# Performance work log

Measured on AMD Instinct MI355X. Metric: run time of the kernel, lower is better.

## Reference

```python
import jax, jax.numpy as jnp
import numpy as np
from jax import lax

LEAK = 0.2   # LeakyReLU negative slope
EPS = 1e-5   # LayerNorm eps (torch default)
K = 16       # nsample

def _lrelu(x):
    return jnp.where(x > 0, x, LEAK * x)

def _ln(x, g, b):
    m = x.mean(-1, keepdims=True)
    v = x.var(-1, keepdims=True)
    return (x - m) / jnp.sqrt(v + EPS) * g + b

def _pointconv(xyz, new_xyz, feats, W, b):
    # xyz [B,N,3], new_xyz [B,M,3], feats [B,N,C] -> [B,M,O]
    d2 = (jnp.sum(new_xyz**2, -1)[:, :, None]
          + jnp.sum(xyz**2, -1)[:, None, :]
          - 2.0 * jnp.einsum('bmd,bnd->bmn', new_xyz, xyz))   # [B,M,N]
    _, idx = lax.top_k(-d2, K)                                # kNN indices [B,M,K]
    bidx = jnp.arange(xyz.shape[0])[:, None, None]
    g_xyz = xyz[bidx, idx] - new_xyz[:, :, None, :]           # relative coords [B,M,K,3]
    g_f = feats[bidx, idx]                                    # neighbor feats  [B,M,K,C]
    g = jnp.concatenate([g_xyz, g_f], -1)                     # [B,M,K,C+3]
    h = _lrelu(jnp.einsum('bmkc,co->bmko', g, W) + b)         # local MLP
    return h.max(2)                                           # max-pool over neighbors

def setup_inputs():
    key = jax.random.key(0)
    ks = jax.random.split(key, 8)
    B, N, base, C1 = 256, 1024, 16, 32
    def w(k, shape, fan):
        return jax.random.normal(k, shape, jnp.float32) * (1.0 / np.sqrt(fan))
    return dict(
        point_cloud=jax.random.normal(ks[0], (B, 3, N), jnp.float32),
        pw_W0=w(ks[1], (3, base), 3), pw_b0=jnp.zeros(base), pw_g0=jnp.ones(base), pw_beta0=jnp.zeros(base),
        pw_W1=w(ks[2], (base, base), base), pw_b1=jnp.zeros(base), pw_g1=jnp.ones(base), pw_beta1=jnp.zeros(base),
        pc0_W=w(ks[3], (base + 3, C1), base + 3), pc0_b=jnp.zeros(C1),
        bn_Ws=w(ks[4], (C1, C1 // 4), C1), bn_bs=jnp.zeros(C1 // 4),
        bn_Wc=w(ks[5], (C1 // 4 + 3, 128), C1 // 4 + 3), bn_bc=jnp.zeros(128),
        bn_We=w(ks[6], (128, 256), 128), bn_be=jnp.zeros(256),
    )

def reference(point_cloud, pw_W0, pw_b0, pw_g0, pw_beta0, pw_W1, pw_b1, pw_g1, pw_beta1,
              pc0_W, pc0_b, bn_Ws, bn_bs, bn_Wc, bn_bc, bn_We, bn_be):
    xyz0 = jnp.swapaxes(point_cloud, 1, 2)   # [B,1024,3]
    xyz1 = xyz0[:, ::2]                      # strided downsample -> [B,512,3]
    xyz2 = xyz1[:, ::4]                      # -> [B,128,3]
    # pointwise MLP (Linear-LN-LeakyReLU x2)
    f = _lrelu(_ln(xyz0 @ pw_W0 + pw_b0, pw_g0, pw_beta0))
    f = _lrelu(_ln(f @ pw_W1 + pw_b1, pw_g1, pw_beta1))       # [B,1024,16]
    # PointConv layer 0: 1024 -> 512 points, 16 -> 32 ch
    f = _pointconv(xyz0, xyz1, f, pc0_W, pc0_b)               # [B,512,32]
    # BottleneckStridedPointConv: squeeze (32->8), grouped conv (->128), expand (->256)
    fs = _lrelu(f @ bn_Ws + bn_bs)                            # [B,512,8]
    f = _pointconv(xyz1, xyz2, fs, bn_Wc, bn_bc)              # [B,128,128]
    f = f @ bn_We + bn_be                                     # [B,128,256]
    return f.mean(1)                                          # mean over points -> [B,256]
```

## Files before the change

kernel.cpp:

```cpp
#include <hip/hip_runtime.h>
#include <float.h>
#include <math.h>

#define LEAK 0.2f
#define EPS 1e-5f

__device__ __forceinline__ float lrelu(float v){ return v > 0.f ? v : LEAK*v; }

__device__ __forceinline__ void ln_lrelu16(float* h, const float* __restrict__ g, const float* __restrict__ be){
  float mu = 0.f;
#pragma unroll
  for (int o=0;o<16;o++) mu += h[o];
  mu *= 0.0625f;
  float var = 0.f;
#pragma unroll
  for (int o=0;o<16;o++){ float d = h[o]-mu; var += d*d; }
  var *= 0.0625f;
  float rs = 1.0f / sqrtf(var + EPS);
#pragma unroll
  for (int o=0;o<16;o++){ float v = (h[o]-mu)*rs*g[o] + be[o]; h[o] = lrelu(v); }
}

__global__ __launch_bounds__(256) void prep_kernel(const float* __restrict__ pc,
    const float* __restrict__ W0, const float* __restrict__ b0, const float* __restrict__ g0, const float* __restrict__ be0,
    const float* __restrict__ W1, const float* __restrict__ b1, const float* __restrict__ g1, const float* __restrict__ be1,
    float4* __restrict__ cand, float* __restrict__ feats)
{
  const int p = blockIdx.x*256 + threadIdx.x;
  const int b = p >> 10, n = p & 1023;
  const float* base = pc + b*3072;
  const float x = base[n], y = base[1024+n], z = base[2048+n];
  cand[p] = make_float4(x, y, z, x*x + y*y + z*z);
  float h[16];
#pragma unroll
  for (int o=0;o<16;o++) h[o] = b0[o] + x*W0[o] + y*W0[16+o] + z*W0[32+o];
  ln_lrelu16(h, g0, be0);
  float h2[16];
#pragma unroll
  for (int o=0;o<16;o++){
    float s = b1[o];
#pragma unroll
    for (int c=0;c<16;c++) s += h[c]*W1[c*16+o];
    h2[o] = s;
  }
  ln_lrelu16(h2, g1, be1);
  float4* fo = (float4*)(feats + p*16);
  fo[0] = make_float4(h2[0],h2[1],h2[2],h2[3]);
  fo[1] = make_float4(h2[4],h2[5],h2[6],h2[7]);
  fo[2] = make_float4(h2[8],h2[9],h2[10],h2[11]);
  fo[3] = make_float4(h2[12],h2[13],h2[14],h2[15]);
}

#define KNN_SENT 0xFF7FFC00u
__device__ __forceinline__ unsigned enc_key(float d, int n){
  unsigned u = __float_as_uint(d);
  u ^= (unsigned)(((int)u) >> 31) | 0x80000000u;
  return (u & ~1023u) | (unsigned)n;
}
__device__ __forceinline__ float dec_key(unsigned k){
  unsigned u = k ^ ((unsigned)(~(((int)k) >> 31)) | 0x80000000u);
  return __uint_as_float(u);
}

__device__ __forceinline__ unsigned med3u(unsigned a, unsigned b, unsigned c){
  unsigned d;
  asm("v_med3_u32 %0, %1, %2, %3" : "=v"(d) : "v"(a), "v"(b), "v"(c));
  return d;
}

__device__ __forceinline__ void ins_sorted(unsigned (&dk)[16], unsigned key){
#pragma unroll
  for (int j=15;j>0;--j) dk[j] = med3u(dk[j-1], dk[j], key);
  dk[0] = key < dk[0] ? key : dk[0];
}

template<int QS, int CS, int NQTOT, int NQ, int SPLIT, int NCAND>
__device__ __forceinline__ void knn_body(const float4* __restrict__ cand, int* __restrict__ idx_out)
{
  constexpr int NC = NCAND / SPLIT;
  constexpr int QG = NQTOT / NQ;
  constexpr int W  = SPLIT*NQ;
  constexpr int QSL = QS / CS;
  __shared__ unsigned md[16*W];
  __shared__ float4 scand[NCAND];
  const int b = blockIdx.x / QG, qg = blockIdx.x % QG;
  const int tid = threadIdx.x;
  const int m = tid & (NQ-1), s = tid / NQ;
  const int mg = qg*NQ + m;
  const float4* __restrict__ cb = cand + b*1024;

  for (int i = tid; i < NCAND; i += NQ*SPLIT)
    scand[i] = cb[i*CS];
  __syncthreads();

  const float4 qv = scand[mg*QSL];
  const float qx2=-2.f*qv.x, qy2=-2.f*qv.y, qz2=-2.f*qv.z;
  const int n0u = __builtin_amdgcn_readfirstlane(s*NC);

  unsigned dk[16];
#pragma unroll
  for (int j=0;j<16;j++) dk[j] = KNN_SENT;

#pragma unroll
  for (int t=0;t<16;t++){
    float4 c = scand[n0u+t];
    float d = fmaf(c.x,qx2, fmaf(c.y,qy2, fmaf(c.z,qz2, c.w)));
    ins_sorted(dk, enc_key(d, n0u+t));
  }
  float Tf = dec_key(dk[15]);

  for (int ch=0; ch<NC/64; ch++){
    const int cb0u = n0u + ch*64;
    unsigned long long msk = 0ull;
    if (ch == 0){
#pragma unroll
      for (int t=16;t<64;t++){
        float4 c = scand[cb0u+t];
        float d = fmaf(c.x,qx2, fmaf(c.y,qy2, fmaf(c.z,qz2, c.w)));
        if (d < Tf) msk |= (1ull<<t);
      }
    } else {
#pragma unroll 16
      for (int t=0;t<64;t++){
        float4 c = scand[cb0u+t];
        float d = fmaf(c.x,qx2, fmaf(c.y,qy2, fmaf(c.z,qz2, c.w)));
        if (d < Tf) msk |= (1ull<<t);
      }
    }
    while (msk){
      const int t = __builtin_ctzll(msk);
      msk &= msk-1ull;
      float4 c = scand[cb0u+t];
      float d = fmaf(c.x,qx2, fmaf(c.y,qy2, fmaf(c.z,qz2, c.w)));
      ins_sorted(dk, enc_key(d, cb0u+t));
    }
    Tf = dec_key(dk[15]);
  }

  if (s > 0){
    const int col = s*NQ + m;
#pragma unroll
    for (int j=0;j<16;j++) md[j*W + col] = dk[j];
  }
#pragma unroll
  for (int step = SPLIT/2; step > 1; step >>= 1){
    __syncthreads();
    if (s < step){
      const int col2 = (s+step)*NQ + m;
#pragma unroll
      for (int j=0;j<16;j++) ins_sorted(dk, md[j*W + col2]);
      if (s > 0){
        const int col = s*NQ + m;
#pragma unroll
        for (int j=0;j<16;j++) md[j*W + col] = dk[j];
      }
    }
  }
  __syncthreads();
  if (s == 0){
    const int col2 = NQ + m;
#pragma unroll
    for (int j=0;j<16;j++){
      unsigned o = md[(15-j)*W + col2];
      dk[j] = o < dk[j] ? o : dk[j];
    }
    int ik[16];
#pragma unroll
    for (int j=0;j<16;j++) ik[j] = (int)(dk[j] & 1023u);
    int4* op = (int4*)(idx_out + (b*NQTOT + mg)*16);
    op[0] = make_int4(ik[0],ik[1],ik[2],ik[3]);
    op[1] = make_int4(ik[4],ik[5],ik[6],ik[7]);
    op[2] = make_int4(ik[8],ik[9],ik[10],ik[11]);
    op[3] = make_int4(ik[12],ik[13],ik[14],ik[15]);
  }
}

__global__ __attribute__((amdgpu_flat_work_group_size(1024,1024), amdgpu_waves_per_eu(4,4)))
void knn1_kernel(const float4* __restrict__ cand, int* __restrict__ idx_out){
  knn_body<2,1,512,512,2,1024>(cand, idx_out);
}
__global__ __attribute__((amdgpu_flat_work_group_size(1024,1024), amdgpu_waves_per_eu(4,4)))
void knn2_kernel(const float4* __restrict__ cand, int* __restrict__ idx_out){
  knn_body<8,2,128,128,8,512>(cand, idx_out);
}

__global__ __attribute__((amdgpu_flat_work_group_size(512,512), amdgpu_waves_per_eu(4,4)))
void feat1_kernel(const float4* __restrict__ cand,
    const float* __restrict__ feats, const int* __restrict__ idx1,
    const float* __restrict__ W, const float* __restrict__ Wb,
    const float* __restrict__ Ws,
    float* __restrict__ p1part)
{
  __shared__ float sPT[16*1024];
  __shared__ float sx[1024], sy[1024], sz[1024];
  const int bx = blockIdx.x;
  const int b = bx >> 1, ob = bx & 1;
  const int ob16 = ob*16;
  const int tid = threadIdx.x;
  const float4* __restrict__ cb = cand + b*1024;
  { float4 c0 = cb[tid], c1 = cb[tid+512];
    sx[tid]=c0.x; sy[tid]=c0.y; sz[tid]=c0.z;
    sx[tid+512]=c1.x; sy[tid+512]=c1.y; sz[tid+512]=c1.z; }

  const float4* __restrict__ fb4 = (const float4*)(feats + b*16384);
#pragma unroll
  for (int i=0;i<2;i++){
    const int j = tid + i*512;
    float4 f0 = fb4[j*4+0], f1 = fb4[j*4+1], f2 = fb4[j*4+2], f3 = fb4[j*4+3];
    float f[16] = {f0.x,f0.y,f0.z,f0.w, f1.x,f1.y,f1.z,f1.w,
                   f2.x,f2.y,f2.z,f2.w, f3.x,f3.y,f3.z,f3.w};
#pragma unroll
    for (int o4=0;o4<4;o4++){
      float4 s = *(const float4*)(Wb + ob16 + o4*4);
#pragma unroll
      for (int c=0;c<16;c++){
        float4 w = *(const float4*)(W + (3+c)*32 + ob16 + o4*4);
        s.x = fmaf(f[c], w.x, s.x);
        s.y = fmaf(f[c], w.y, s.y);
        s.z = fmaf(f[c], w.z, s.z);
        s.w = fmaf(f[c], w.w, s.w);
      }
      sPT[(o4*4+0)*1024 + j] = s.x;
      sPT[(o4*4+1)*1024 + j] = s.y;
      sPT[(o4*4+2)*1024 + j] = s.z;
      sPT[(o4*4+3)*1024 + j] = s.w;
    }
  }
  __syncthreads();

  const int m = tid;
  const float qx = sx[2*m], qy = sy[2*m], qz = sz[2*m];
  int idxr[16];
  { const int4* ip = (const int4*)(idx1 + (b*512+m)*16);
    int4 a=ip[0], b2=ip[1], c2=ip[2], d2=ip[3];
    idxr[0]=a.x; idxr[1]=a.y; idxr[2]=a.z; idxr[3]=a.w;
    idxr[4]=b2.x; idxr[5]=b2.y; idxr[6]=b2.z; idxr[7]=b2.w;
    idxr[8]=c2.x; idxr[9]=c2.y; idxr[10]=c2.z; idxr[11]=c2.w;
    idxr[12]=d2.x; idxr[13]=d2.y; idxr[14]=d2.z; idxr[15]=d2.w; }

  float w0[16], w1[16], w2[16];
#pragma unroll
  for (int i=0;i<4;i++){
    float4 a = *(const float4*)(W +       ob16 + i*4);
    float4 bb= *(const float4*)(W + 32  + ob16 + i*4);
    float4 cc= *(const float4*)(W + 64  + ob16 + i*4);
    w0[i*4]=a.x; w0[i*4+1]=a.y; w0[i*4+2]=a.z; w0[i*4+3]=a.w;
    w1[i*4]=bb.x; w1[i*4+1]=bb.y; w1[i*4+2]=bb.z; w1[i*4+3]=bb.w;
    w2[i*4]=cc.x; w2[i*4+1]=cc.y; w2[i*4+2]=cc.z; w2[i*4+3]=cc.w;
  }

  float acc[16];
#pragma unroll
  for (int o=0;o<16;o++) acc[o] = -FLT_MAX;

#pragma unroll 4
  for (int k=0;k<16;k++){
    const int j = idxr[k];
    const float gx = sx[j]-qx, gy = sy[j]-qy, gz = sz[j]-qz;
    const float* pj = sPT + j;
#pragma unroll
    for (int o=0;o<16;o++){
      float p = pj[o*1024];
      float h = fmaf(gz, w2[o], fmaf(gy, w1[o], fmaf(gx, w0[o], p)));
      acc[o] = fmaxf(acc[o], fmaxf(h, 0.2f*h));
    }
  }

  float fsacc[8] = {0.f,0.f,0.f,0.f,0.f,0.f,0.f,0.f};
#pragma unroll
  for (int o=0;o<16;o++){
    const float a = acc[o];
    float4 u = *(const float4*)(Ws + (ob16+o)*8);
    float4 v = *(const float4*)(Ws + (ob16+o)*8 + 4);
    fsacc[0] = fmaf(a, u.x, fsacc[0]);
    fsacc[1] = fmaf(a, u.y, fsacc[1]);
    fsacc[2] = fmaf(a, u.z, fsacc[2]);
    fsacc[3] = fmaf(a, u.w, fsacc[3]);
    fsacc[4] = fmaf(a, v.x, fsacc[4]);
    fsacc[5] = fmaf(a, v.y, fsacc[5]);
    fsacc[6] = fmaf(a, v.z, fsacc[6]);
    fsacc[7] = fmaf(a, v.w, fsacc[7]);
  }
  float4* op = (float4*)(p1part + ((b*2+ob)*512 + m)*8);
  op[0] = make_float4(fsacc[0],fsacc[1],fsacc[2],fsacc[3]);
  op[1] = make_float4(fsacc[4],fsacc[5],fsacc[6],fsacc[7]);
}

__global__ __attribute__((amdgpu_flat_work_group_size(512,512), amdgpu_waves_per_eu(4,4)))
void feat2_kernel(const float4* __restrict__ cand,
    const float* __restrict__ p1part, const int* __restrict__ idx2,
    const float* __restrict__ Wc, const float* __restrict__ bc,
    const float* __restrict__ bs,
    float* __restrict__ p2red)
{
  __shared__ float sP2[512*32];
  __shared__ float sx[512], sy[512], sz[512];
  __shared__ float sred[32];
  const int bx = blockIdx.x;
  const int b = bx >> 2, ob = bx & 3;
  const int o_base = ob*32;
  const int tid = threadIdx.x;

  const float4* __restrict__ cb = cand + b*1024;
  { float4 c0 = cb[2*tid];
    sx[tid]=c0.x; sy[tid]=c0.y; sz[tid]=c0.z; }
  if (tid < 32) sred[tid] = 0.f;

  { const float4* __restrict__ pa4 = (const float4*)(p1part + ((b*2+0)*512 + tid)*8);
    const float4* __restrict__ pb4 = (const float4*)(p1part + ((b*2+1)*512 + tid)*8);
    float4 a0 = pa4[0], a1 = pa4[1], c0 = pb4[0], c1 = pb4[1];
    float4 s0 = *(const float4*)(bs), s1 = *(const float4*)(bs+4);
    float f[8];
    f[0]=lrelu(a0.x+c0.x+s0.x); f[1]=lrelu(a0.y+c0.y+s0.y);
    f[2]=lrelu(a0.z+c0.z+s0.z); f[3]=lrelu(a0.w+c0.w+s0.w);
    f[4]=lrelu(a1.x+c1.x+s1.x); f[5]=lrelu(a1.y+c1.y+s1.y);
    f[6]=lrelu(a1.z+c1.z+s1.z); f[7]=lrelu(a1.w+c1.w+s1.w);
    float* row = sP2 + tid*32;
    const int sw = (tid & 7);
#pragma unroll
    for (int o4=0;o4<8;o4++){
      float4 s = *(const float4*)(bc + o_base + o4*4);
#pragma unroll
      for (int c=0;c<8;c++){
        float4 w = *(const float4*)(Wc + (3+c)*128 + o_base + o4*4);
        s.x = fmaf(f[c], w.x, s.x);
        s.y = fmaf(f[c], w.y, s.y);
        s.z = fmaf(f[c], w.z, s.z);
        s.w = fmaf(f[c], w.w, s.w);
      }
      *(float4*)(row + ((o4 ^ sw) << 2)) = s;
    }
  }
  __syncthreads();

  const int m = tid >> 2, oq = tid & 3;
  const float qx = sx[4*m], qy = sy[4*m], qz = sz[4*m];
  int idxr[16];
  { const int4* ip = (const int4*)(idx2 + (b*128+m)*16);
    int4 a=ip[0], b2=ip[1], c2=ip[2], d2=ip[3];
    idxr[0]=a.x; idxr[1]=a.y; idxr[2]=a.z; idxr[3]=a.w;
    idxr[4]=b2.x; idxr[5]=b2.y; idxr[6]=b2.z; idxr[7]=b2.w;
    idxr[8]=c2.x; idxr[9]=c2.y; idxr[10]=c2.z; idxr[11]=c2.w;
    idxr[12]=d2.x; idxr[13]=d2.y; idxr[14]=d2.z; idxr[15]=d2.w; }

  float w0[8], w1[8], w2[8];
  { const int og = o_base + oq*8;
#pragma unroll
    for (int i=0;i<2;i++){
      float4 a = *(const float4*)(Wc +        og + i*4);
      float4 bb= *(const float4*)(Wc + 128  + og + i*4);
      float4 cc= *(const float4*)(Wc + 256  + og + i*4);
      w0[i*4]=a.x; w0[i*4+1]=a.y; w0[i*4+2]=a.z; w0[i*4+3]=a.w;
      w1[i*4]=bb.x; w1[i*4+1]=bb.y; w1[i*4+2]=bb.z; w1[i*4+3]=bb.w;
      w2[i*4]=cc.x; w2[i*4+1]=cc.y; w2[i*4+2]=cc.z; w2[i*4+3]=cc.w;
    } }

  float acc[8];
#pragma unroll
  for (int o=0;o<8;o++) acc[o] = -FLT_MAX;

#pragma unroll 4
  for (int k=0;k<16;k++){
    const int j = idxr[k];
    const float gx = sx[j]-qx, gy = sy[j]-qy, gz = sz[j]-qz;
    const float* row = sP2 + j*32;
    const int sw = (j & 7);
    float4 p0 = *(const float4*)(row + (((2*oq  ) ^ sw) << 2));
    float4 p1 = *(const float4*)(row + (((2*oq+1) ^ sw) << 2));
    float h0 = fmaf(gz, w2[0], fmaf(gy, w1[0], fmaf(gx, w0[0], p0.x)));
    float h1 = fmaf(gz, w2[1], fmaf(gy, w1[1], fmaf(gx, w0[1], p0.y)));
    float h2 = fmaf(gz, w2[2], fmaf(gy, w1[2], fmaf(gx, w0[2], p0.z)));
    float h3 = fmaf(gz, w2[3], fmaf(gy, w1[3], fmaf(gx, w0[3], p0.w)));
    float h4 = fmaf(gz, w2[4], fmaf(gy, w1[4], fmaf(gx, w0[4], p1.x)));
    float h5 = fmaf(gz, w2[5], fmaf(gy, w1[5], fmaf(gx, w0[5], p1.y)));
    float h6 = fmaf(gz, w2[6], fmaf(gy, w1[6], fmaf(gx, w0[6], p1.z)));
    float h7 = fmaf(gz, w2[7], fmaf(gy, w1[7], fmaf(gx, w0[7], p1.w)));
    acc[0] = fmaxf(acc[0], fmaxf(h0, 0.2f*h0));
    acc[1] = fmaxf(acc[1], fmaxf(h1, 0.2f*h1));
    acc[2] = fmaxf(acc[2], fmaxf(h2, 0.2f*h2));
    acc[3] = fmaxf(acc[3], fmaxf(h3, 0.2f*h3));
    acc[4] = fmaxf(acc[4], fmaxf(h4, 0.2f*h4));
    acc[5] = fmaxf(acc[5], fmaxf(h5, 0.2f*h5));
    acc[6] = fmaxf(acc[6], fmaxf(h6, 0.2f*h6));
    acc[7] = fmaxf(acc[7], fmaxf(h7, 0.2f*h7));
  }

#pragma unroll
  for (int o=0;o<8;o++){
    float v = acc[o];
    v += __shfl_xor(v, 4);
    v += __shfl_xor(v, 8);
    v += __shfl_xor(v, 16);
    v += __shfl_xor(v, 32);
    if ((threadIdx.x & 60) == 0)
      atomicAdd(&sred[oq*8+o], v);
  }
  __syncthreads();
  if (tid < 32) p2red[b*128 + o_base + tid] = sred[tid];
}

__global__ __launch_bounds__(256) void final_kernel(const float* __restrict__ p2red,
    const float* __restrict__ We, const float* __restrict__ beF, float* __restrict__ out)
{
  const int b = blockIdx.x, o = threadIdx.x;
  const float* __restrict__ r0 = p2red + b*128;
  float s = 0.f;
#pragma unroll 8
  for (int c=0;c<128;c++) s += r0[c]*We[c*256+o];
  out[b*256+o] = beF[o] + s*0.0078125f;
}

extern "C" void kernel_launch(void* const* d_in, const int* in_sizes, int n_in,
                              void* d_out, int out_size, void* d_ws, size_t ws_size,
                              hipStream_t stream) {
  (void)in_sizes; (void)n_in; (void)out_size; (void)ws_size;
  const float* pc   = (const float*)d_in[0];
  const float* W0   = (const float*)d_in[1];
  const float* b0   = (const float*)d_in[2];
  const float* g0   = (const float*)d_in[3];
  const float* be0  = (const float*)d_in[4];
  const float* W1   = (const float*)d_in[5];
  const float* b1   = (const float*)d_in[6];
  const float* g1   = (const float*)d_in[7];
  const float* be1  = (const float*)d_in[8];
  const float* pcW  = (const float*)d_in[9];
  const float* pcb  = (const float*)d_in[10];
  const float* Ws   = (const float*)d_in[11];
  const float* bs   = (const float*)d_in[12];
  const float* Wc   = (const float*)d_in[13];
  const float* bc   = (const float*)d_in[14];
  const float* We   = (const float*)d_in[15];
  const float* beF  = (const float*)d_in[16];

  char* ws = (char*)d_ws;
  float4* cand0 = (float4*)ws;
  float*  feats = (float*)(ws + (4u<<20));
  float*  p2red = (float*)(ws + (4u<<20));
  int*    idx1  = (int*)  (ws + (20u<<20));
  int*    idx2  = (int*)  (ws + (28u<<20));
  float*  p1part= (float*)(ws + (30u<<20));
  float*  out   = (float*)d_out;

  prep_kernel<<<1024, 256, 0, stream>>>(pc, W0,b0,g0,be0, W1,b1,g1,be1, cand0, feats);
  knn1_kernel<<<256, 1024, 0, stream>>>(cand0, idx1);
  knn2_kernel<<<256, 1024, 0, stream>>>(cand0, idx2);
  feat1_kernel<<<512, 512, 0, stream>>>(cand0, feats, idx1, pcW, pcb, Ws, p1part);
  feat2_kernel<<<1024, 512, 0, stream>>>(cand0, p1part, idx2, Wc, bc, bs, p2red);
  final_kernel<<<256, 256, 0, stream>>>(p2red, We, beF, out);
}
```

Measured before the change: 238.5 us.

## Fuse both kNN launches into one kernel and seed top-k with 64 candidates

Merges the two kNN kernels into a single 512-block launch that dispatches by block index, sharing one statically sized LDS buffer. This removes a launch boundary and lets the two workloads run concurrently to fill the GPU. It also seeds the sorted list with the first 64 candidates via full insertion instead of 16 plus a mask pass, and relaxes the waves-per-EU hint. The shared 80KB LDS allocation is larger than what knn2 needed alone, which may reduce occupancy for those blocks. The longer seeding phase also adds insertion work.

Measured after the change: 213.5 us. 10.5% less time.

```diff
diff --git a/kernel.cpp b/kernel.cpp
--- a/kernel.cpp
+++ b/kernel.cpp
@@ -75,15 +75,14 @@
 }
 
 template<int QS, int CS, int NQTOT, int NQ, int SPLIT, int NCAND>
-__device__ __forceinline__ void knn_body(const float4* __restrict__ cand, int* __restrict__ idx_out)
+__device__ __forceinline__ void knn_body(unsigned* md, float4* scand,
+    const float4* __restrict__ cand, int bid, int* __restrict__ idx_out)
 {
   constexpr int NC = NCAND / SPLIT;
   constexpr int QG = NQTOT / NQ;
   constexpr int W  = SPLIT*NQ;
   constexpr int QSL = QS / CS;
-  __shared__ unsigned md[16*W];
-  __shared__ float4 scand[NCAND];
-  const int b = blockIdx.x / QG, qg = blockIdx.x % QG;
+  const int b = bid / QG, qg = bid % QG;
   const int tid = threadIdx.x;
   const int m = tid & (NQ-1), s = tid / NQ;
   const int mg = qg*NQ + m;
@@ -101,31 +100,22 @@
 #pragma unroll
   for (int j=0;j<16;j++) dk[j] = KNN_SENT;
 
-#pragma unroll
-  for (int t=0;t<16;t++){
+#pragma unroll 8
+  for (int t=0;t<64;t++){
     float4 c = scand[n0u+t];
     float d = fmaf(c.x,qx2, fmaf(c.y,qy2, fmaf(c.z,qz2, c.w)));
     ins_sorted(dk, enc_key(d, n0u+t));
   }
   float Tf = dec_key(dk[15]);
 
-  for (int ch=0; ch<NC/64; ch++){
+  for (int ch=1; ch<NC/64; ch++){
     const int cb0u = n0u + ch*64;
     unsigned long long msk = 0ull;
-    if (ch == 0){
-#pragma unroll
-      for (int t=16;t<64;t++){
-        float4 c = scand[cb0u+t];
-        float d = fmaf(c.x,qx2, fmaf(c.y,qy2, fmaf(c.z,qz2, c.w)));
-        if (d < Tf) msk |= (1ull<<t);
-      }
-    } else {
 #pragma unroll 16
-      for (int t=0;t<64;t++){
-        float4 c = scand[cb0u+t];
-        float d = fmaf(c.x,qx2, fmaf(c.y,qy2, fmaf(c.z,qz2, c.w)));
-        if (d < Tf) msk |= (1ull<<t);
-      }
+    for (int t=0;t<64;t++){
+      float4 c = scand[cb0u+t];
+      float d = fmaf(c.x,qx2, fmaf(c.y,qy2, fmaf(c.z,qz2, c.w)));
+      if (d < Tf) msk |= (1ull<<t);
     }
     while (msk){
       const int t = __builtin_ctzll(msk);
@@ -175,13 +165,20 @@
   }
 }
 
-__global__ __attribute__((amdgpu_flat_work_group_size(1024,1024), amdgpu_waves_per_eu(4,4)))
-void knn1_kernel(const float4* __restrict__ cand, int* __restrict__ idx_out){
-  knn_body<2,1,512,512,2,1024>(cand, idx_out);
-}
-__global__ __attribute__((amdgpu_flat_work_group_size(1024,1024), amdgpu_waves_per_eu(4,4)))
-void knn2_kernel(const float4* __restrict__ cand, int* __restrict__ idx_out){
-  knn_body<8,2,128,128,8,512>(cand, idx_out);
+__global__ __attribute__((amdgpu_flat_work_group_size(1024,1024), amdgpu_waves_per_eu(4,8)))
+void knn_fused_kernel(const float4* __restrict__ cand,
+                      int* __restrict__ idx1, int* __restrict__ idx2)
+{
+  __shared__ __align__(16) char smem[81920];
+  unsigned* md   = (unsigned*)smem;
+  float4** dummy = nullptr; (void)dummy;
+  if (blockIdx.x < 256){
+    float4* scand = (float4*)(smem + 65536);
+    knn_body<2,1,512,512,2,1024>(md, scand, cand, blockIdx.x, idx1);
+  } else {
+    float4* scand = (float4*)(smem + 65536);
+    knn_body<8,2,128,128,8,512>(md, scand, cand, blockIdx.x - 256, idx2);
+  }
 }
 
 __global__ __attribute__((amdgpu_flat_work_group_size(512,512), amdgpu_waves_per_eu(4,4)))
@@ -442,8 +439,7 @@
   float*  out   = (float*)d_out;
 
   prep_kernel<<<1024, 256, 0, stream>>>(pc, W0,b0,g0,be0, W1,b1,g1,be1, cand0, feats);
-  knn1_kernel<<<256, 1024, 0, stream>>>(cand0, idx1);
-  knn2_kernel<<<256, 1024, 0, stream>>>(cand0, idx2);
+  knn_fused_kernel<<<512, 1024, 0, stream>>>(cand0, idx1, idx2);
   feat1_kernel<<<512, 512, 0, stream>>>(cand0, feats, idx1, pcW, pcb, Ws, p1part);
   feat2_kernel<<<1024, 512, 0, stream>>>(cand0, p1part, idx2, Wc, bc, bs, p2red);
   final_kernel<<<256, 256, 0, stream>>>(p2red, We, beF, out);
```
